# Performance work log

Hardware: AMD Instinct MI355X
Metric: run time of the kernel (lower is better)

Reference implementation:

```python
import jax, jax.numpy as jnp
import numpy as np

D, HID, NH, L, T, B = 512, 2048, 8, 4, 32, 16


def _pe(length, dim):
    pos = jnp.arange(length, dtype=jnp.float32)[:, None]
    div = jnp.exp(jnp.arange(0, dim, 2, dtype=jnp.float32) * (-np.log(10000.0) / dim))
    pe = jnp.zeros((length, dim), dtype=jnp.float32)
    pe = pe.at[:, 0::2].set(jnp.sin(pos * div)).at[:, 1::2].set(jnp.cos(pos * div))
    return pe[None]  # [1, length, dim]


def _ln(x, g, b, eps=1e-5):
    m = x.mean(-1, keepdims=True)
    v = ((x - m) ** 2).mean(-1, keepdims=True)
    return (x - m) * jax.lax.rsqrt(v + eps) * g + b


def _mha(xq, xkv, w, b, ow, ob):
    # torch MultiheadAttention: packed in_proj weight [3D, D], out_proj [D, D]
    d = xq.shape[-1]
    hd = d // NH
    q = xq @ w[:d].T + b[:d]
    k = xkv @ w[d:2 * d].T + b[d:2 * d]
    v = xkv @ w[2 * d:].T + b[2 * d:]
    sp = lambda t: t.reshape(t.shape[0], t.shape[1], NH, hd)
    att = jnp.einsum('bqhd,bkhd->bhqk', sp(q), sp(k)) / np.sqrt(hd)
    att = jax.nn.softmax(att, axis=-1)
    o = jnp.einsum('bhqk,bkhd->bqhd', att, sp(v))
    return o.reshape(o.shape[0], o.shape[1], d) @ ow.T + ob


def _ffn(x, w1, b1, w2, b2):
    return jax.nn.gelu(x @ w1.T + b1, approximate=False) @ w2.T + b2


def setup_inputs():
    key = jax.random.key(0)
    kit = iter(jax.random.split(key, 64))
    rn = lambda shape, s=0.02: jax.random.normal(next(kit), shape, dtype=jnp.float32) * s
    z = lambda shape: jnp.zeros(shape, jnp.float32)
    o = lambda shape: jnp.ones(shape, jnp.float32)
    inp = dict(y=jax.random.normal(next(kit), (B, D), dtype=jnp.float32),
               start_vec=rn((1, 1, D), 1.0), target_length=T)
    inp.update(enc_qkv_w=rn((L, 3 * D, D)), enc_qkv_b=z((L, 3 * D)), enc_out_w=rn((L, D, D)), enc_out_b=z((L, D)),
               enc_ff1_w=rn((L, HID, D)), enc_ff1_b=z((L, HID)), enc_ff2_w=rn((L, D, HID)), enc_ff2_b=z((L, D)),
               enc_ln1_g=o((L, D)), enc_ln1_b=z((L, D)), enc_ln2_g=o((L, D)), enc_ln2_b=z((L, D)),
               enc_lnf_g=o((D,)), enc_lnf_b=z((D,)),
               dec_qkv_w=rn((L, 3 * D, D)), dec_qkv_b=z((L, 3 * D)), dec_out_w=rn((L, D, D)), dec_out_b=z((L, D)),
               dec_x_qkv_w=rn((L, 3 * D, D)), dec_x_qkv_b=z((L, 3 * D)), dec_x_out_w=rn((L, D, D)), dec_x_out_b=z((L, D)),
               dec_ff1_w=rn((L, HID, D)), dec_ff1_b=z((L, HID)), dec_ff2_w=rn((L, D, HID)), dec_ff2_b=z((L, D)),
               dec_ln1_g=o((L, D)), dec_ln1_b=z((L, D)), dec_ln2_g=o((L, D)), dec_ln2_b=z((L, D)),
               dec_ln3_g=o((L, D)), dec_ln3_b=z((L, D)), dec_lnf_g=o((D,)), dec_lnf_b=z((D,)))
    return inp


def reference(y, start_vec, enc_qkv_w, enc_qkv_b, enc_out_w, enc_out_b, enc_ff1_w, enc_ff1_b, enc_ff2_w, enc_ff2_b,
              enc_ln1_g, enc_ln1_b, enc_ln2_g, enc_ln2_b, enc_lnf_g, enc_lnf_b,
              dec_qkv_w, dec_qkv_b, dec_out_w, dec_out_b, dec_x_qkv_w, dec_x_qkv_b, dec_x_out_w, dec_x_out_b,
              dec_ff1_w, dec_ff1_b, dec_ff2_w, dec_ff2_b,
              dec_ln1_g, dec_ln1_b, dec_ln2_g, dec_ln2_b, dec_ln3_g, dec_ln3_b, dec_lnf_g, dec_lnf_b,
              target_length):
    Bsz, Dm = y.shape
    pe = _pe(target_length, Dm)
    # encoder: src seq_len = 1; encoder output is identical every step, compute once
    x = y[:, None, :] + pe[:, :1]
    for i in range(L):
        x = _ln(x + _mha(x, x, enc_qkv_w[i], enc_qkv_b[i], enc_out_w[i], enc_out_b[i]), enc_ln1_g[i], enc_ln1_b[i])
        x = _ln(x + _ffn(x, enc_ff1_w[i], enc_ff1_b[i], enc_ff2_w[i], enc_ff2_b[i]), enc_ln2_g[i], enc_ln2_b[i])
    mem = _ln(x, enc_lnf_g, enc_lnf_b)
    tgt = jnp.tile(start_vec, (Bsz, 1, 1))
    for _ in range(target_length):
        h = tgt + pe[:, :tgt.shape[1]]
        for i in range(L):
            h = _ln(h + _mha(h, h, dec_qkv_w[i], dec_qkv_b[i], dec_out_w[i], dec_out_b[i]), dec_ln1_g[i], dec_ln1_b[i])
            h = _ln(h + _mha(h, mem, dec_x_qkv_w[i], dec_x_qkv_b[i], dec_x_out_w[i], dec_x_out_b[i]), dec_ln2_g[i], dec_ln2_b[i])
            h = _ln(h + _ffn(h, dec_ff1_w[i], dec_ff1_b[i], dec_ff2_w[i], dec_ff2_b[i]), dec_ln3_g[i], dec_ln3_b[i])
        h = _ln(h, dec_lnf_g, dec_lnf_b)
        tgt = jnp.concatenate([tgt, h[:, -1:, :]], axis=1)
    return tgt[:, 1:, :]
```

## Files before the change

### kernel.cpp

```cpp
#include <hip/hip_runtime.h>
#include <math.h>


#define NB 128
#define NT 512
#define GM 8
#define NGRP 16
#define Dm 512
#define HIDN 2048
#define TLEN 32
#define BSZ 16
#define NLAY 4
#define PBF 147968

typedef unsigned int uint32;
typedef unsigned short u16;
typedef short bf16x8 __attribute__((ext_vector_type(8)));
typedef float f32x4 __attribute__((ext_vector_type(4)));

struct Params {
  const float* y; const float* start;
  const float *eqw, *eqb, *eow, *eob, *ef1w, *ef1b, *ef2w, *ef2b;
  const float *eln1g, *eln1b, *eln2g, *eln2b, *elnfg, *elnfb;
  const float *dqw, *dqb, *dow, *dob, *dxqw, *dxqb, *dxow, *dxob;
  const float *df1w, *df1b, *df2w, *df2b;
  const float *dln1g, *dln1b, *dln2g, *dln2b, *dln3g, *dln3b, *dlnfg, *dlnfb;
  float* out; float* ws;
};

__device__ __forceinline__ u16 f2b(float x) {
  uint32 u = __float_as_uint(x);
  u += 0x7fffu + ((u >> 16) & 1u);
  return (u16)(u >> 16);
}
__device__ __forceinline__ float dot4f(float4 a, float4 b) {
  return a.x*b.x + a.y*b.y + a.z*b.z + a.w*b.w;
}

struct DecS {
  u16 P[8][512];
  u16 Ob[16][520];
  float Of[16][516];
};
struct EncS { float xn[2048]; };
union Smem { DecS d; EncS e; };

__device__ __forceinline__ void wave_ln(float v[8], const float* __restrict__ g,
                                        const float* __restrict__ bt, int cb) {
  float sum = 0.f, sq = 0.f;
#pragma unroll
  for (int q = 0; q < 8; ++q) { sum += v[q]; sq += v[q]*v[q]; }
#pragma unroll
  for (int m = 32; m; m >>= 1) { sum += __shfl_xor(sum, m, 64); sq += __shfl_xor(sq, m, 64); }
  float mean = sum * (1.f/Dm);
  float var  = sq  * (1.f/Dm) - mean*mean;
  float rs = rsqrtf(var + 1e-5f);
#pragma unroll
  for (int q = 0; q < 8; ++q) v[q] = (v[q]-mean)*rs*g[cb+q] + bt[cb+q];
}

template<int K>
__device__ __forceinline__ void wave_gemm(const u16* __restrict__ A,
                                          const u16* __restrict__ W, f32x4 acc[4]) {
  const int lane = threadIdx.x & 63;
  const int l15 = lane & 15, kg = lane >> 4;
  const u16* a = A + (size_t)l15*K + kg*8;
  const u16* w = W + (size_t)l15*K + kg*8;
#pragma unroll 4
  for (int kc = 0; kc < K/32; ++kc) {
    bf16x8 av = *(const bf16x8*)(a + kc*32);
#pragma unroll
    for (int cg = 0; cg < 4; ++cg) {
      bf16x8 bv = *(const bf16x8*)(w + (size_t)cg*16*K + kc*32);
      acc[cg] = __builtin_amdgcn_mfma_f32_16x16x32_bf16(av, bv, acc[cg], 0, 0, 0);
    }
  }
}

__device__ __forceinline__ float dotn(const float* __restrict__ xn,
                                      const float* __restrict__ w, int n4) {
  const float4* x4 = (const float4*)xn;
  const float4* w4 = (const float4*)w;
  float a = 0.f;
#pragma unroll 8
  for (int k = 0; k < n4; ++k) a += dot4f(x4[k], w4[k]);
  return a;
}

__device__ void convw(const float* __restrict__ s, u16* __restrict__ d, int n,
                      int gtid, int gs) {
  const float2* s2 = (const float2*)s;
  uint32* d2 = (uint32*)d;
  for (int i = gtid; i < n/2; i += gs) {
    float2 v = s2[i];
    d2[i] = (uint32)f2b(v.x) | ((uint32)f2b(v.y) << 16);
  }
}

#define BAR(cp, n, ep) do {                                                       \
    __syncthreads();                                                              \
    if (t == 0) {                                                                 \
      __hip_atomic_fetch_add((cp), 1u, __ATOMIC_RELEASE, __HIP_MEMORY_SCOPE_AGENT);\
      ++(ep);                                                                     \
      unsigned tg_ = (ep) * (unsigned)(n);                                        \
      while (__hip_atomic_load((cp), __ATOMIC_RELAXED, __HIP_MEMORY_SCOPE_AGENT) < tg_) \
        __builtin_amdgcn_s_sleep(2);                                              \
      (void)__hip_atomic_load((cp), __ATOMIC_ACQUIRE, __HIP_MEMORY_SCOPE_AGENT);  \
    }                                                                             \
    __syncthreads();                                                              \
  } while (0)

__global__ __launch_bounds__(NT) void ar_transformer(Params p) {
  __shared__ Smem sm;
  const int bid = blockIdx.x;
  const int t = threadIdx.x;
  const int g = bid & 15;
  const int m = bid >> 4;
  const int b = g;
  const int wv = t >> 6, lane = t & 63, cb = lane * 8;
  const int l15 = lane & 15, kg = lane >> 4;
  unsigned epA = 0, epG = 0;

  unsigned* cbase = (unsigned*)p.ws;
  unsigned* cntA = cbase;
  unsigned* cntG = cbase + 16 + g*16;
  float* f = p.ws + 1024;
  float* pe = f;            f += TLEN*Dm;
  float* batch0 = f;        f += (size_t)NGRP * PBF;
  u16* wq16 = (u16*)f;
  u16* wo16 = wq16 + (size_t)NLAY*1536*512;
  u16* w116 = wo16 + (size_t)NLAY*512*512;
  u16* w216 = w116 + (size_t)NLAY*2048*512;

  float* bb = batch0 + (size_t)b * PBF;
  float* xrow = bb, *arow = bb+512, *ofrow = bb+1024, *h2row = bb+1536, *frow = bb+2048;
  float* urow = bb+2560, *vxall = bb+4608, *crossE = bb+6656;
  float* h0f = bb+8704, *hf = bb+25088, *h2f = bb+41472;
  u16* ub16 = (u16*)(bb + 57856);
  u16* h0b  = ub16;
  u16* hb   = h0b + 16384;
  u16* h2b  = hb + 16384;
  u16* qkvb = h2b + 16384;
  u16* ubuf = qkvb + 49152;
  u16* vt   = ubuf + 65536;

  const int gtid = bid*NT + t, gs = NB*NT;

  convw(p.dqw,  wq16, NLAY*1536*512, gtid, gs);
  convw(p.dow,  wo16, NLAY*512*512,  gtid, gs);
  convw(p.df1w, w116, NLAY*2048*512, gtid, gs);
  convw(p.df2w, w216, NLAY*512*2048, gtid, gs);
  for (int i = gtid; i < TLEN*Dm; i += gs) {
    int tt = i >> 9, d = i & (Dm-1);
    int half = d >> 1;
    float ang = (float)tt * expf(-(float)(2*half) * (9.210340371976184f/512.0f));
    pe[i] = (d & 1) ? cosf(ang) : sinf(ang);
  }
  for (int i = gtid; i < BSZ*Dm; i += gs) {
    int bI = i >> 9, c = i & (Dm-1);
    float* bbI = batch0 + (size_t)bI*PBF;
    bbI[c] = p.y[i] + ((c & 1) ? 1.0f : 0.0f);
    float v0 = p.start[c] + ((c & 1) ? 1.0f : 0.0f);
    bbI[8704 + c] = v0;
    ((u16*)(bbI + 57856))[c] = f2b(v0);
  }
  BAR(cntA, NB, epA);

  for (int l = 0; l < NLAY; ++l) {
    if (l == 0) {
      for (int i = t; i < 512; i += NT) sm.e.xn[i] = xrow[i];
    } else if (wv == 0) {
      float v[8];
#pragma unroll
      for (int q = 0; q < 8; ++q) v[q] = h2row[cb+q] + frow[cb+q];
      wave_ln(v, p.eln2g + (l-1)*Dm, p.eln2b + (l-1)*Dm, cb);
#pragma unroll
      for (int q = 0; q < 8; ++q) sm.e.xn[cb+q] = v[q];
      if (m == 0)
#pragma unroll
        for (int q = 0; q < 8; ++q) xrow[cb+q] = v[q];
    }
    __syncthreads();
    if (t < 64) {
      int c = m*64 + t;
      arow[c] = dotn(sm.e.xn, p.eqw + ((size_t)l*1536 + 1024 + c)*512, 128)
                + p.eqb[l*1536 + 1024 + c];
    }
    BAR(cntG, GM, epG);
    for (int i = t; i < 512; i += NT) sm.e.xn[i] = arow[i];
    __syncthreads();
    if (t < 64) {
      int c = m*64 + t;
      ofrow[c] = dotn(sm.e.xn, p.eow + ((size_t)l*512 + c)*512, 128) + p.eob[l*512 + c];
    }
    BAR(cntG, GM, epG);
    if (wv == 0) {
      float v[8];
#pragma unroll
      for (int q = 0; q < 8; ++q) v[q] = xrow[cb+q] + ofrow[cb+q];
      wave_ln(v, p.eln1g + l*Dm, p.eln1b + l*Dm, cb);
#pragma unroll
      for (int q = 0; q < 8; ++q) sm.e.xn[cb+q] = v[q];
      if (m == 0)
#pragma unroll
        for (int q = 0; q < 8; ++q) h2row[cb+q] = v[q];
    }
    __syncthreads();
    if (t < 256) {
      int c = m*256 + t;
      float u = dotn(sm.e.xn, p.ef1w + ((size_t)l*2048 + c)*512, 128) + p.ef1b[l*2048 + c];
      u = 0.5f*u*(1.0f + erff(u*0.70710678118654752f));
      urow[c] = u;
    }
    BAR(cntG, GM, epG);
    for (int i = t; i < 2048; i += NT) sm.e.xn[i] = urow[i];
    __syncthreads();
    if (t < 64) {
      int c = m*64 + t;
      frow[c] = dotn(sm.e.xn, p.ef2w + ((size_t)l*512 + c)*2048, 512) + p.ef2b[l*512 + c];
    }
    BAR(cntG, GM, epG);
  }
  if (wv == 0) {
    float v[8];
#pragma unroll
    for (int q = 0; q < 8; ++q) v[q] = h2row[cb+q] + frow[cb+q];
    wave_ln(v, p.eln2g + 3*Dm, p.eln2b + 3*Dm, cb);
    wave_ln(v, p.elnfg, p.elnfb, cb);
#pragma unroll
    for (int q = 0; q < 8; ++q) sm.e.xn[cb+q] = v[q];
  }
  __syncthreads();
  if (t < 256) {
    int cc = m*256 + t, lc = cc >> 9, c = cc & 511;
    vxall[cc] = dotn(sm.e.xn, p.dxqw + ((size_t)lc*1536 + 1024 + c)*512, 128)
                + p.dxqb[lc*1536 + 1024 + c];
  }
  BAR(cntG, GM, epG);
  for (int i = t; i < 2048; i += NT) sm.e.xn[i] = vxall[i];
  __syncthreads();
  if (t < 256) {
    int cc = m*256 + t, lc = cc >> 9, c = cc & 511;
    crossE[cc] = dotn(sm.e.xn + lc*512, p.dxow + ((size_t)lc*512 + c)*512, 128)
                 + p.dxob[lc*512 + c];
  }
  BAR(cntG, GM, epG);

  for (int st = 0; st < TLEN; ++st) {
    const int s = st + 1;
    const int JT = (s + 15) >> 4;
    const int jtL = (s - 1) >> 4;
    for (int l = 0; l < NLAY; ++l) {
      {
        const u16* Asrc = (l == 0) ? h0b : hb;
        int ntile = JT*24, tid = m*8 + wv;
        if (tid < ntile) {
          int jt = tid/24, c24 = tid%24, c0 = c24*64;
          f32x4 acc[4] = {};
          wave_gemm<512>(Asrc + (size_t)jt*16*512, wq16 + ((size_t)l*1536 + c0)*512, acc);
#pragma unroll
          for (int cg = 0; cg < 4; ++cg) {
            int col = c0 + cg*16 + l15;
            float bias = p.dqb[l*1536 + col];
#pragma unroll
            for (int r = 0; r < 4; ++r) {
              int j = jt*16 + kg*4 + r;
              if (j < s) {
                float v = acc[cg][r] + bias;
                if (col < 512)       qkvb[(size_t)j*1536 + col] = f2b(v * 0.125f);
                else if (col < 1024) qkvb[(size_t)j*1536 + col] = f2b(v);
                else {
                  int d = col - 1024;
                  vt[(size_t)((d >> 6)*64 + (d & 63))*32 + j] = f2b(v);
                }
              }
            }
          }
        }
      }
      BAR(cntG, GM, epG);
      {
        bool act; int jt;
        if (l == NLAY-1) { act = (m == 0); jt = jtL; }
        else             { act = (m < JT); jt = m;   }
        if (act) {
          const int h = wv;
          f32x4 sc[2] = {};
          const u16* qA = qkvb + (size_t)(jt*16 + l15)*1536 + h*64 + kg*8;
          const u16* kB = qkvb + 512 + h*64 + kg*8;
#pragma unroll
          for (int ks = 0; ks < 2; ++ks) {
            bf16x8 av = *(const bf16x8*)(qA + ks*32);
#pragma unroll
            for (int cg = 0; cg < 2; ++cg) {
              bf16x8 bv = *(const bf16x8*)(kB + (size_t)(cg*16 + l15)*1536 + ks*32);
              sc[cg] = __builtin_amdgcn_mfma_f32_16x16x32_bf16(av, bv, sc[cg], 0, 0, 0);
            }
          }
#pragma unroll
          for (int r = 0; r < 4; ++r) {
            float v0 = (l15      < s) ? sc[0][r] : -3.0e38f;
            float v1 = (l15 + 16 < s) ? sc[1][r] : -3.0e38f;
            float mx = fmaxf(v0, v1);
#pragma unroll
            for (int mk = 1; mk < 16; mk <<= 1) mx = fmaxf(mx, __shfl_xor(mx, mk, 64));
            float e0 = expf(v0 - mx), e1 = expf(v1 - mx);
            float sum = e0 + e1;
#pragma unroll
            for (int mk = 1; mk < 16; mk <<= 1) sum += __shfl_xor(sum, mk, 64);
            float inv = 1.0f / sum;
            int row = kg*4 + r;
            sm.d.P[h][row*32 + l15]      = f2b(e0 * inv);
            sm.d.P[h][row*32 + 16 + l15] = f2b(e1 * inv);
          }
          __syncthreads();
          f32x4 ov[4] = {};
          bf16x8 pa = *(const bf16x8*)&sm.d.P[h][l15*32 + kg*8];
#pragma unroll
          for (int cg = 0; cg < 4; ++cg) {
            bf16x8 bv = *(const bf16x8*)(vt + (size_t)(h*64 + cg*16 + l15)*32 + kg*8);
            ov[cg] = __builtin_amdgcn_mfma_f32_16x16x32_bf16(pa, bv, ov[cg], 0, 0, 0);
          }
#pragma unroll
          for (int cg = 0; cg < 4; ++cg)
#pragma unroll
            for (int r = 0; r < 4; ++r)
              sm.d.Ob[kg*4 + r][h*64 + cg*16 + l15] = f2b(ov[cg][r]);
          __syncthreads();
          f32x4 oc[4] = {};
          int c0 = wv*64;
          const u16* wB = wo16 + ((size_t)l*512 + c0 + l15)*512 + kg*8;
#pragma unroll 4
          for (int ks = 0; ks < 16; ++ks) {
            bf16x8 av = *(const bf16x8*)&sm.d.Ob[l15][kg*8 + ks*32];
#pragma unroll
            for (int cg = 0; cg < 4; ++cg) {
              bf16x8 bv = *(const bf16x8*)(wB + (size_t)cg*16*512 + ks*32);
              oc[cg] = __builtin_amdgcn_mfma_f32_16x16x32_bf16(av, bv, oc[cg], 0, 0, 0);
            }
          }
#pragma unroll
          for (int cg = 0; cg < 4; ++cg) {
            int col = c0 + cg*16 + l15;
            float bias = p.dob[l*512 + col];
#pragma unroll
            for (int r = 0; r < 4; ++r)
              sm.d.Of[kg*4 + r][col] = oc[cg][r] + bias;
          }
          __syncthreads();
          const float* xin = (l == 0) ? h0f : hf;
          for (int jr = wv; jr < 16; jr += 8) {
            int j = jt*16 + jr;
            float v[8];
#pragma unroll
            for (int q = 0; q < 8; ++q) v[q] = xin[(size_t)j*512 + cb+q] + sm.d.Of[jr][cb+q];
            wave_ln(v, p.dln1g + l*512, p.dln1b + l*512, cb);
#pragma unroll
            for (int q = 0; q < 8; ++q) v[q] += crossE[l*512 + cb+q];
            wave_ln(v, p.dln2g + l*512, p.dln2b + l*512, cb);
            if (j < s) {
#pragma unroll
              for (int q = 0; q < 8; ++q) {
                h2f[(size_t)j*512 + cb+q] = v[q];
                h2b[(size_t)j*512 + cb+q] = f2b(v[q]);
              }
            }
          }
        }
      }
      BAR(cntG, GM, epG);
      {
        int ntile = (l == NLAY-1) ? 32 : JT*32;
        int tid = m*8 + wv;
        if (tid < ntile) {
          int jt, c;
          if (l == NLAY-1) { jt = jtL; c = tid; } else { jt = tid >> 5; c = tid & 31; }
          f32x4 acc[4] = {};
          wave_gemm<512>(h2b + (size_t)jt*16*512, w116 + ((size_t)l*2048 + c*64)*512, acc);
#pragma unroll
          for (int cg = 0; cg < 4; ++cg) {
            int col = c*64 + cg*16 + l15;
            float bias = p.df1b[l*2048 + col];
#pragma unroll
            for (int r = 0; r < 4; ++r) {
              int j = jt*16 + kg*4 + r;
              if (j < s) {
                float u = acc[cg][r] + bias;
                u = 0.5f*u*(1.0f + erff(u*0.70710678118654752f));
                ubuf[(size_t)j*2048 + col] = f2b(u);
              }
            }
          }
        }
      }
      BAR(cntG, GM, epG);
      {
        bool act; int jt;
        if (l == NLAY-1) { act = (m == 0); jt = jtL; }
        else             { act = (m < JT); jt = m;   }
        if (act) {
          f32x4 acc[4] = {};
          int c0 = wv*64;
          wave_gemm<2048>(ubuf + (size_t)jt*16*2048, w216 + ((size_t)l*512 + c0)*2048, acc);
#pragma unroll
          for (int cg = 0; cg < 4; ++cg) {
            int col = c0 + cg*16 + l15;
            float bias = p.df2b[l*512 + col];
#pragma unroll
            for (int r = 0; r < 4; ++r)
              sm.d.Of[kg*4 + r][col] = acc[cg][r] + bias;
          }
          __syncthreads();
          for (int jr = wv; jr < 16; jr += 8) {
            int j = jt*16 + jr;
            float v[8];
#pragma unroll
            for (int q = 0; q < 8; ++q) v[q] = h2f[(size_t)j*512 + cb+q] + sm.d.Of[jr][cb+q];
            wave_ln(v, p.dln3g + l*512, p.dln3b + l*512, cb);
            if (j < s) {
#pragma unroll
              for (int q = 0; q < 8; ++q) {
                hf[(size_t)j*512 + cb+q] = v[q];
                hb[(size_t)j*512 + cb+q] = f2b(v[q]);
              }
            }
            if (l == NLAY-1 && j == s-1) {
              wave_ln(v, p.dlnfg, p.dlnfb, cb);
#pragma unroll
              for (int q = 0; q < 8; ++q) {
                float ov = v[q];
                p.out[(size_t)(b*TLEN + st)*512 + cb+q] = ov;
                if (st + 1 < TLEN) {
                  float nh = ov + pe[(size_t)(st+1)*512 + cb+q];
                  h0f[(size_t)(st+1)*512 + cb+q] = nh;
                  h0b[(size_t)(st+1)*512 + cb+q] = f2b(nh);
                }
              }
            }
          }
        }
      }
      BAR(cntG, GM, epG);
    }
  }
}

extern "C" void kernel_launch(void* const* d_in, const int* in_sizes, int n_in,
                              void* d_out, int out_size, void* d_ws, size_t ws_size,
                              hipStream_t stream) {
  Params P;
  P.y     = (const float*)d_in[0];
  P.start = (const float*)d_in[1];
  P.eqw  = (const float*)d_in[3];  P.eqb  = (const float*)d_in[4];
  P.eow  = (const float*)d_in[5];  P.eob  = (const float*)d_in[6];
  P.ef1w = (const float*)d_in[7];  P.ef1b = (const float*)d_in[8];
  P.ef2w = (const float*)d_in[9];  P.ef2b = (const float*)d_in[10];
  P.eln1g = (const float*)d_in[11]; P.eln1b = (const float*)d_in[12];
  P.eln2g = (const float*)d_in[13]; P.eln2b = (const float*)d_in[14];
  P.elnfg = (const float*)d_in[15]; P.elnfb = (const float*)d_in[16];
  P.dqw  = (const float*)d_in[17]; P.dqb  = (const float*)d_in[18];
  P.dow  = (const float*)d_in[19]; P.dob  = (const float*)d_in[20];
  P.dxqw = (const float*)d_in[21]; P.dxqb = (const float*)d_in[22];
  P.dxow = (const float*)d_in[23]; P.dxob = (const float*)d_in[24];
  P.df1w = (const float*)d_in[25]; P.df1b = (const float*)d_in[26];
  P.df2w = (const float*)d_in[27]; P.df2b = (const float*)d_in[28];
  P.dln1g = (const float*)d_in[29]; P.dln1b = (const float*)d_in[30];
  P.dln2g = (const float*)d_in[31]; P.dln2b = (const float*)d_in[32];
  P.dln3g = (const float*)d_in[33]; P.dln3b = (const float*)d_in[34];
  P.dlnfg = (const float*)d_in[35]; P.dlnfb = (const float*)d_in[36];
  P.out = (float*)d_out;
  P.ws  = (float*)d_ws;
  hipMemsetAsync(d_ws, 0, 4096, stream);
  hipLaunchKernelGGL(ar_transformer, dim3(NB), dim3(NT), 0, stream, P);
}
```

Baseline: 22.31 ms.

## Run one 1024-thread block per batch row and drop inter-block grid barriers

The kernel moves from 128 blocks (8 cooperating blocks per batch row, synchronized with atomic counter barriers) to 16 blocks of 1024 threads, one per batch row. All per-step stages then sync with __syncthreads only. The GEMM helper is changed so each wave handles two 16-row tiles, and the FFN intermediate is kept in LDS. This removes the cost of the global barriers but uses an eighth as many CUs, so the weight GEMMs lose a lot of parallelism and each block has to stream all the weights by itself.

```diff
diff --git a/kernel.cpp b/kernel.cpp
--- a/kernel.cpp
+++ b/kernel.cpp
@@ -2,16 +2,13 @@
 #include <math.h>
 
 
-#define NB 128
-#define NT 512
-#define GM 8
-#define NGRP 16
+#define NBLK 16
+#define NT 1024
 #define Dm 512
 #define HIDN 2048
 #define TLEN 32
-#define BSZ 16
 #define NLAY 4
-#define PBF 147968
+#define RSZ 149504
 
 typedef unsigned int uint32;
 typedef unsigned short u16;
@@ -37,12 +34,8 @@
   return a.x*b.x + a.y*b.y + a.z*b.z + a.w*b.w;
 }
 
-struct DecS {
-  u16 P[8][512];
-  u16 Ob[16][520];
-  float Of[16][516];
-};
-struct EncS { float xn[2048]; };
+struct DecS { u16 P[16][16][32]; u16 u[2][16][2056]; };
+struct EncS { float xs[512]; float as[512]; float h2[512]; float fr[512]; float us[2048]; };
 union Smem { DecS d; EncS e; };
 
 __device__ __forceinline__ void wave_ln(float v[8], const float* __restrict__ g,
@@ -60,19 +53,22 @@
 }
 
 template<int K>
-__device__ __forceinline__ void wave_gemm(const u16* __restrict__ A,
-                                          const u16* __restrict__ W, f32x4 acc[4]) {
+__device__ __forceinline__ void wgemm2(const u16* __restrict__ A, int lda, int nj,
+                                       const u16* __restrict__ W, f32x4 acc[2][4]) {
   const int lane = threadIdx.x & 63;
   const int l15 = lane & 15, kg = lane >> 4;
-  const u16* a = A + (size_t)l15*K + kg*8;
-  const u16* w = W + (size_t)l15*K + kg*8;
-#pragma unroll 4
+  const u16* a0 = A + (size_t)l15*lda + kg*8;
+  const u16* a1 = a0 + (size_t)(nj > 1 ? 16 : 0)*lda;
+#pragma unroll 2
   for (int kc = 0; kc < K/32; ++kc) {
-    bf16x8 av = *(const bf16x8*)(a + kc*32);
+    bf16x8 av0 = *(const bf16x8*)(a0 + kc*32);
+    bf16x8 av1 = *(const bf16x8*)(a1 + kc*32);
+    const u16* w = W + (size_t)l15*K + kg*8 + kc*32;
 #pragma unroll
     for (int cg = 0; cg < 4; ++cg) {
-      bf16x8 bv = *(const bf16x8*)(w + (size_t)cg*16*K + kc*32);
-      acc[cg] = __builtin_amdgcn_mfma_f32_16x16x32_bf16(av, bv, acc[cg], 0, 0, 0);
+      bf16x8 bv = *(const bf16x8*)(w + (size_t)cg*16*K);
+      acc[0][cg] = __builtin_amdgcn_mfma_f32_16x16x32_bf16(av0, bv, acc[0][cg], 0, 0, 0);
+      acc[1][cg] = __builtin_amdgcn_mfma_f32_16x16x32_bf16(av1, bv, acc[1][cg], 0, 0, 0);
     }
   }
 }
@@ -97,194 +93,160 @@
   }
 }
 
-#define BAR(cp, n, ep) do {                                                       \
-    __syncthreads();                                                              \
-    if (t == 0) {                                                                 \
-      __hip_atomic_fetch_add((cp), 1u, __ATOMIC_RELEASE, __HIP_MEMORY_SCOPE_AGENT);\
-      ++(ep);                                                                     \
-      unsigned tg_ = (ep) * (unsigned)(n);                                        \
-      while (__hip_atomic_load((cp), __ATOMIC_RELAXED, __HIP_MEMORY_SCOPE_AGENT) < tg_) \
-        __builtin_amdgcn_s_sleep(2);                                              \
-      (void)__hip_atomic_load((cp), __ATOMIC_ACQUIRE, __HIP_MEMORY_SCOPE_AGENT);  \
-    }                                                                             \
-    __syncthreads();                                                              \
-  } while (0)
-
 __global__ __launch_bounds__(NT) void ar_transformer(Params p) {
   __shared__ Smem sm;
   const int bid = blockIdx.x;
+  const int b = bid;
   const int t = threadIdx.x;
-  const int g = bid & 15;
-  const int m = bid >> 4;
-  const int b = g;
   const int wv = t >> 6, lane = t & 63, cb = lane * 8;
   const int l15 = lane & 15, kg = lane >> 4;
-  unsigned epA = 0, epG = 0;
-
-  unsigned* cbase = (unsigned*)p.ws;
-  unsigned* cntA = cbase;
-  unsigned* cntG = cbase + 16 + g*16;
-  float* f = p.ws + 1024;
-  float* pe = f;            f += TLEN*Dm;
-  float* batch0 = f;        f += (size_t)NGRP * PBF;
-  u16* wq16 = (u16*)f;
+
+  unsigned* cnt = (unsigned*)p.ws;
+  u16* wq16 = (u16*)(p.ws + 256);
   u16* wo16 = wq16 + (size_t)NLAY*1536*512;
   u16* w116 = wo16 + (size_t)NLAY*512*512;
   u16* w216 = w116 + (size_t)NLAY*2048*512;
-
-  float* bb = batch0 + (size_t)b * PBF;
-  float* xrow = bb, *arow = bb+512, *ofrow = bb+1024, *h2row = bb+1536, *frow = bb+2048;
-  float* urow = bb+2560, *vxall = bb+4608, *crossE = bb+6656;
-  float* h0f = bb+8704, *hf = bb+25088, *h2f = bb+41472;
-  u16* ub16 = (u16*)(bb + 57856);
-  u16* h0b  = ub16;
+  float* bat0 = (float*)(w216 + (size_t)NLAY*512*2048);
+
+  float* bb   = bat0 + (size_t)b * RSZ;
+  float* pe   = bb;
+  float* h0f  = bb + 16384;
+  float* hf   = bb + 32768;
+  float* h2f  = bb + 49152;
+  float* ofb  = bb + 65536;
+  float* crossE = bb + 81920;
+  u16* h0b  = (u16*)(bb + 83968);
   u16* hb   = h0b + 16384;
   u16* h2b  = hb + 16384;
   u16* qkvb = h2b + 16384;
-  u16* ubuf = qkvb + 49152;
-  u16* vt   = ubuf + 65536;
-
-  const int gtid = bid*NT + t, gs = NB*NT;
+  u16* vt   = qkvb + 49152;
+  u16* obb  = vt + 16384;
+
+  const int gtid = bid*NT + t, gs = NBLK*NT;
 
   convw(p.dqw,  wq16, NLAY*1536*512, gtid, gs);
   convw(p.dow,  wo16, NLAY*512*512,  gtid, gs);
   convw(p.df1w, w116, NLAY*2048*512, gtid, gs);
   convw(p.df2w, w216, NLAY*512*2048, gtid, gs);
-  for (int i = gtid; i < TLEN*Dm; i += gs) {
+  for (int i = t; i < TLEN*Dm; i += NT) {
     int tt = i >> 9, d = i & (Dm-1);
     int half = d >> 1;
     float ang = (float)tt * expf(-(float)(2*half) * (9.210340371976184f/512.0f));
     pe[i] = (d & 1) ? cosf(ang) : sinf(ang);
   }
-  for (int i = gtid; i < BSZ*Dm; i += gs) {
-    int bI = i >> 9, c = i & (Dm-1);
-    float* bbI = batch0 + (size_t)bI*PBF;
-    bbI[c] = p.y[i] + ((c & 1) ? 1.0f : 0.0f);
-    float v0 = p.start[c] + ((c & 1) ? 1.0f : 0.0f);
-    bbI[8704 + c] = v0;
-    ((u16*)(bbI + 57856))[c] = f2b(v0);
-  }
-  BAR(cntA, NB, epA);
+  if (t < 512) {
+    float v0 = p.start[t] + ((t & 1) ? 1.0f : 0.0f);
+    h0f[t] = v0; h0b[t] = f2b(v0);
+  }
+  __syncthreads();
+  if (t == 0) {
+    __hip_atomic_fetch_add(cnt, 1u, __ATOMIC_RELEASE, __HIP_MEMORY_SCOPE_AGENT);
+    while (__hip_atomic_load(cnt, __ATOMIC_RELAXED, __HIP_MEMORY_SCOPE_AGENT) < (unsigned)NBLK)
+      __builtin_amdgcn_s_sleep(2);
+    (void)__hip_atomic_load(cnt, __ATOMIC_ACQUIRE, __HIP_MEMORY_SCOPE_AGENT);
+  }
+  __syncthreads();
 
   for (int l = 0; l < NLAY; ++l) {
     if (l == 0) {
-      for (int i = t; i < 512; i += NT) sm.e.xn[i] = xrow[i];
+      if (t < 512) sm.e.xs[t] = p.y[(size_t)b*512 + t] + ((t & 1) ? 1.0f : 0.0f);
     } else if (wv == 0) {
       float v[8];
 #pragma unroll
-      for (int q = 0; q < 8; ++q) v[q] = h2row[cb+q] + frow[cb+q];
+      for (int q = 0; q < 8; ++q) v[q] = sm.e.h2[cb+q] + sm.e.fr[cb+q];
       wave_ln(v, p.eln2g + (l-1)*Dm, p.eln2b + (l-1)*Dm, cb);
 #pragma unroll
-      for (int q = 0; q < 8; ++q) sm.e.xn[cb+q] = v[q];
-      if (m == 0)
-#pragma unroll
-        for (int q = 0; q < 8; ++q) xrow[cb+q] = v[q];
+      for (int q = 0; q < 8; ++q) sm.e.xs[cb+q] = v[q];
     }
     __syncthreads();
-    if (t < 64) {
-      int c = m*64 + t;
-      arow[c] = dotn(sm.e.xn, p.eqw + ((size_t)l*1536 + 1024 + c)*512, 128)
-                + p.eqb[l*1536 + 1024 + c];
-    }
-    BAR(cntG, GM, epG);
-    for (int i = t; i < 512; i += NT) sm.e.xn[i] = arow[i];
-    __syncthreads();
-    if (t < 64) {
-      int c = m*64 + t;
-      ofrow[c] = dotn(sm.e.xn, p.eow + ((size_t)l*512 + c)*512, 128) + p.eob[l*512 + c];
-    }
-    BAR(cntG, GM, epG);
+    if (t < 512)
+      sm.e.as[t] = dotn(sm.e.xs, p.eqw + ((size_t)l*1536 + 1024 + t)*512, 128)
+                   + p.eqb[l*1536 + 1024 + t];
+    __syncthreads();
+    if (t < 512)
+      sm.e.fr[t] = dotn(sm.e.as, p.eow + ((size_t)l*512 + t)*512, 128) + p.eob[l*512 + t];
+    __syncthreads();
     if (wv == 0) {
       float v[8];
 #pragma unroll
-      for (int q = 0; q < 8; ++q) v[q] = xrow[cb+q] + ofrow[cb+q];
+      for (int q = 0; q < 8; ++q) v[q] = sm.e.xs[cb+q] + sm.e.fr[cb+q];
       wave_ln(v, p.eln1g + l*Dm, p.eln1b + l*Dm, cb);
 #pragma unroll
-      for (int q = 0; q < 8; ++q) sm.e.xn[cb+q] = v[q];
-      if (m == 0)
-#pragma unroll
-        for (int q = 0; q < 8; ++q) h2row[cb+q] = v[q];
+      for (int q = 0; q < 8; ++q) sm.e.h2[cb+q] = v[q];
     }
     __syncthreads();
-    if (t < 256) {
-      int c = m*256 + t;
-      float u = dotn(sm.e.xn, p.ef1w + ((size_t)l*2048 + c)*512, 128) + p.ef1b[l*2048 + c];
-      u = 0.5f*u*(1.0f + erff(u*0.70710678118654752f));
-      urow[c] = u;
+    for (int c = t; c < 2048; c += NT) {
+      float u = dotn(sm.e.h2, p.ef1w + ((size_t)l*2048 + c)*512, 128) + p.ef1b[l*2048 + c];
+      sm.e.us[c] = 0.5f*u*(1.0f + erff(u*0.70710678118654752f));
     }
-    BAR(cntG, GM, epG);
-    for (int i = t; i < 2048; i += NT) sm.e.xn[i] = urow[i];
-    __syncthreads();
-    if (t < 64) {
-      int c = m*64 + t;
-      frow[c] = dotn(sm.e.xn, p.ef2w + ((size_t)l*512 + c)*2048, 512) + p.ef2b[l*512 + c];
-    }
-    BAR(cntG, GM, epG);
+    __syncthreads();
+    if (t < 512)
+      sm.e.fr[t] = dotn(sm.e.us, p.ef2w + ((size_t)l*512 + t)*2048, 512) + p.ef2b[l*512 + t];
+    __syncthreads();
   }
   if (wv == 0) {
     float v[8];
 #pragma unroll
-    for (int q = 0; q < 8; ++q) v[q] = h2row[cb+q] + frow[cb+q];
+    for (int q = 0; q < 8; ++q) v[q] = sm.e.h2[cb+q] + sm.e.fr[cb+q];
     wave_ln(v, p.eln2g + 3*Dm, p.eln2b + 3*Dm, cb);
     wave_ln(v, p.elnfg, p.elnfb, cb);
 #pragma unroll
-    for (int q = 0; q < 8; ++q) sm.e.xn[cb+q] = v[q];
+    for (int q = 0; q < 8; ++q) sm.e.xs[cb+q] = v[q];
   }
   __syncthreads();
-  if (t < 256) {
-    int cc = m*256 + t, lc = cc >> 9, c = cc & 511;
-    vxall[cc] = dotn(sm.e.xn, p.dxqw + ((size_t)lc*1536 + 1024 + c)*512, 128)
-                + p.dxqb[lc*1536 + 1024 + c];
-  }
-  BAR(cntG, GM, epG);
-  for (int i = t; i < 2048; i += NT) sm.e.xn[i] = vxall[i];
+  for (int c = t; c < 2048; c += NT) {
+    int lc = c >> 9, cc = c & 511;
+    sm.e.us[c] = dotn(sm.e.xs, p.dxqw + ((size_t)lc*1536 + 1024 + cc)*512, 128)
+                 + p.dxqb[lc*1536 + 1024 + cc];
+  }
   __syncthreads();
-  if (t < 256) {
-    int cc = m*256 + t, lc = cc >> 9, c = cc & 511;
-    crossE[cc] = dotn(sm.e.xn + lc*512, p.dxow + ((size_t)lc*512 + c)*512, 128)
-                 + p.dxob[lc*512 + c];
-  }
-  BAR(cntG, GM, epG);
+  for (int c = t; c < 2048; c += NT) {
+    int lc = c >> 9, cc = c & 511;
+    crossE[c] = dotn(sm.e.us + lc*512, p.dxow + ((size_t)lc*512 + cc)*512, 128)
+                + p.dxob[lc*512 + cc];
+  }
+  __syncthreads();
 
   for (int st = 0; st < TLEN; ++st) {
     const int s = st + 1;
     const int JT = (s + 15) >> 4;
     const int jtL = (s - 1) >> 4;
     for (int l = 0; l < NLAY; ++l) {
-      {
-        const u16* Asrc = (l == 0) ? h0b : hb;
-        int ntile = JT*24, tid = m*8 + wv;
-        if (tid < ntile) {
-          int jt = tid/24, c24 = tid%24, c0 = c24*64;
-          f32x4 acc[4] = {};
-          wave_gemm<512>(Asrc + (size_t)jt*16*512, wq16 + ((size_t)l*1536 + c0)*512, acc);
+      const int RT0 = (l == NLAY-1) ? jtL : 0;
+      const int RN  = (l == NLAY-1) ? 1 : JT;
+      const u16* Asrc = (l == 0) ? h0b : hb;
+
+      for (int it = wv; it < 24; it += 16) {
+        int c0 = it*64;
+        f32x4 acc[2][4];
+#pragma unroll
+        for (int a2 = 0; a2 < 2; ++a2)
+#pragma unroll
+          for (int cg = 0; cg < 4; ++cg) acc[a2][cg] = (f32x4){0.f,0.f,0.f,0.f};
+        wgemm2<512>(Asrc, 512, JT, wq16 + ((size_t)l*1536 + c0)*512, acc);
+        for (int jl = 0; jl < JT; ++jl)
 #pragma unroll
           for (int cg = 0; cg < 4; ++cg) {
             int col = c0 + cg*16 + l15;
             float bias = p.dqb[l*1536 + col];
 #pragma unroll
             for (int r = 0; r < 4; ++r) {
-              int j = jt*16 + kg*4 + r;
+              int j = jl*16 + kg*4 + r;
               if (j < s) {
-                float v = acc[cg][r] + bias;
+                float v = acc[jl][cg][r] + bias;
                 if (col < 512)       qkvb[(size_t)j*1536 + col] = f2b(v * 0.125f);
                 else if (col < 1024) qkvb[(size_t)j*1536 + col] = f2b(v);
-                else {
-                  int d = col - 1024;
-                  vt[(size_t)((d >> 6)*64 + (d & 63))*32 + j] = f2b(v);
-                }
+                else                 vt[(size_t)(col-1024)*32 + j] = f2b(v);
               }
             }
           }
-        }
-      }
-      BAR(cntG, GM, epG);
+      }
+      __syncthreads();
+
       {
-        bool act; int jt;
-        if (l == NLAY-1) { act = (m == 0); jt = jtL; }
-        else             { act = (m < JT); jt = m;   }
+        bool act = wv < 8*RN;
+        int h = wv & 7, jt = RT0 + (wv >> 3);
         if (act) {
-          const int h = wv;
           f32x4 sc[2] = {};
           const u16* qA = qkvb + (size_t)(jt*16 + l15)*1536 + h*64 + kg*8;
           const u16* kB = qkvb + 512 + h*64 + kg*8;
@@ -310,12 +272,11 @@
             for (int mk = 1; mk < 16; mk <<= 1) sum += __shfl_xor(sum, mk, 64);
             float inv = 1.0f / sum;
             int row = kg*4 + r;
-            sm.d.P[h][row*32 + l15]      = f2b(e0 * inv);
-            sm.d.P[h][row*32 + 16 + l15] = f2b(e1 * inv);
-          }
-          __syncthreads();
+            sm.d.P[wv][row][l15]      = f2b(e0 * inv);
+            sm.d.P[wv][row][16 + l15] = f2b(e1 * inv);
+          }
           f32x4 ov[4] = {};
-          bf16x8 pa = *(const bf16x8*)&sm.d.P[h][l15*32 + kg*8];
+          bf16x8 pa = *(const bf16x8*)&sm.d.P[wv][l15][kg*8];
 #pragma unroll
           for (int cg = 0; cg < 4; ++cg) {
             bf16x8 bv = *(const bf16x8*)(vt + (size_t)(h*64 + cg*16 + l15)*32 + kg*8);
@@ -325,122 +286,121 @@
           for (int cg = 0; cg < 4; ++cg)
 #pragma unroll
             for (int r = 0; r < 4; ++r)
-              sm.d.Ob[kg*4 + r][h*64 + cg*16 + l15] = f2b(ov[cg][r]);
-          __syncthreads();
-          f32x4 oc[4] = {};
-          int c0 = wv*64;
-          const u16* wB = wo16 + ((size_t)l*512 + c0 + l15)*512 + kg*8;
-#pragma unroll 4
-          for (int ks = 0; ks < 16; ++ks) {
-            bf16x8 av = *(const bf16x8*)&sm.d.Ob[l15][kg*8 + ks*32];
-#pragma unroll
-            for (int cg = 0; cg < 4; ++cg) {
-              bf16x8 bv = *(const bf16x8*)(wB + (size_t)cg*16*512 + ks*32);
-              oc[cg] = __builtin_amdgcn_mfma_f32_16x16x32_bf16(av, bv, oc[cg], 0, 0, 0);
+              obb[(size_t)(jt*16 + kg*4 + r)*512 + h*64 + cg*16 + l15] = f2b(ov[cg][r]);
+        }
+      }
+      __syncthreads();
+
+      for (int it = wv; it < 8*RN; it += 16) {
+        int c0 = (it & 7)*64, jt = RT0 + (it >> 3);
+        f32x4 acc[2][4];
+#pragma unroll
+        for (int a2 = 0; a2 < 2; ++a2)
+#pragma unroll
+          for (int cg = 0; cg < 4; ++cg) acc[a2][cg] = (f32x4){0.f,0.f,0.f,0.f};
+        wgemm2<512>(obb + (size_t)jt*16*512, 512, 1, wo16 + ((size_t)l*512 + c0)*512, acc);
+#pragma unroll
+        for (int cg = 0; cg < 4; ++cg) {
+          int col = c0 + cg*16 + l15;
+          float bias = p.dob[l*512 + col];
+#pragma unroll
+          for (int r = 0; r < 4; ++r)
+            ofb[(size_t)(jt*16 + kg*4 + r)*512 + col] = acc[0][cg][r] + bias;
+        }
+      }
+      __syncthreads();
+
+      {
+        const float* xin = (l == 0) ? h0f : hf;
+        for (int r = wv; r < RN*16; r += 16) {
+          int j = RT0*16 + r;
+          float v[8];
+#pragma unroll
+          for (int q = 0; q < 8; ++q) v[q] = xin[(size_t)j*512 + cb+q] + ofb[(size_t)j*512 + cb+q];
+          wave_ln(v, p.dln1g + l*512, p.dln1b + l*512, cb);
+#pragma unroll
+          for (int q = 0; q < 8; ++q) v[q] += crossE[l*512 + cb+q];
+          wave_ln(v, p.dln2g + l*512, p.dln2b + l*512, cb);
+          if (j < s) {
+#pragma unroll
+            for (int q = 0; q < 8; ++q) {
+              h2f[(size_t)j*512 + cb+q] = v[q];
+              h2b[(size_t)j*512 + cb+q] = f2b(v[q]);
             }
           }
+        }
+      }
+      __syncthreads();
+
+      for (int it = wv; it < 32; it += 16) {
+        int c0 = it*64;
+        f32x4 acc[2][4];
+#pragma unroll
+        for (int a2 = 0; a2 < 2; ++a2)
+#pragma unroll
+          for (int cg = 0; cg < 4; ++cg) acc[a2][cg] = (f32x4){0.f,0.f,0.f,0.f};
+        wgemm2<512>(h2b + (size_t)RT0*16*512, 512, RN, w116 + ((size_t)l*2048 + c0)*512, acc);
+        for (int jl = 0; jl < RN; ++jl)
 #pragma unroll
           for (int cg = 0; cg < 4; ++cg) {
             int col = c0 + cg*16 + l15;
-            float bias = p.dob[l*512 + col];
-#pragma unroll
-            for (int r = 0; r < 4; ++r)
-              sm.d.Of[kg*4 + r][col] = oc[cg][r] + bias;
-          }
-          __syncthreads();
-          const float* xin = (l == 0) ? h0f : hf;
-          for (int jr = wv; jr < 16; jr += 8) {
-            int j = jt*16 + jr;
-            float v[8];
-#pragma unroll
-            for (int q = 0; q < 8; ++q) v[q] = xin[(size_t)j*512 + cb+q] + sm.d.Of[jr][cb+q];
-            wave_ln(v, p.dln1g + l*512, p.dln1b + l*512, cb);
-#pragma unroll
-            for (int q = 0; q < 8; ++q) v[q] += crossE[l*512 + cb+q];
-            wave_ln(v, p.dln2g + l*512, p.dln2b + l*512, cb);
-            if (j < s) {
-#pragma unroll
-              for (int q = 0; q < 8; ++q) {
-                h2f[(size_t)j*512 + cb+q] = v[q];
-                h2b[(size_t)j*512 + cb+q] = f2b(v[q]);
-              }
+            float bias = p.df1b[l*2048 + col];
+#pragma unroll
+            for (int r = 0; r < 4; ++r) {
+              float u = acc[jl][cg][r] + bias;
+              sm.d.u[jl][kg*4 + r][col] = f2b(0.5f*u*(1.0f + erff(u*0.70710678118654752f)));
             }
           }
-        }
-      }
-      BAR(cntG, GM, epG);
-      {
-        int ntile = (l == NLAY-1) ? 32 : JT*32;
-        int tid = m*8 + wv;
-        if (tid < ntile) {
-          int jt, c;
-          if (l == NLAY-1) { jt = jtL; c = tid; } else { jt = tid >> 5; c = tid & 31; }
-          f32x4 acc[4] = {};
-          wave_gemm<512>(h2b + (size_t)jt*16*512, w116 + ((size_t)l*2048 + c*64)*512, acc);
-#pragma unroll
-          for (int cg = 0; cg < 4; ++cg) {
-            int col = c*64 + cg*16 + l15;
-            float bias = p.df1b[l*2048 + col];
-#pragma unroll
-            for (int r = 0; r < 4; ++r) {
-              int j = jt*16 + kg*4 + r;
-              if (j < s) {
-                float u = acc[cg][r] + bias;
-                u = 0.5f*u*(1.0f + erff(u*0.70710678118654752f));
-                ubuf[(size_t)j*2048 + col] = f2b(u);
-              }
-            }
-          }
-        }
-      }
-      BAR(cntG, GM, epG);
-      {
-        bool act; int jt;
-        if (l == NLAY-1) { act = (m == 0); jt = jtL; }
-        else             { act = (m < JT); jt = m;   }
-        if (act) {
-          f32x4 acc[4] = {};
-          int c0 = wv*64;
-          wave_gemm<2048>(ubuf + (size_t)jt*16*2048, w216 + ((size_t)l*512 + c0)*2048, acc);
+      }
+      __syncthreads();
+      for (int it = wv; it < 8; it += 16) {
+        int c0 = it*64;
+        f32x4 acc[2][4];
+#pragma unroll
+        for (int a2 = 0; a2 < 2; ++a2)
+#pragma unroll
+          for (int cg = 0; cg < 4; ++cg) acc[a2][cg] = (f32x4){0.f,0.f,0.f,0.f};
+        wgemm2<2048>((const u16*)&sm.d.u[0][0][0], 2056, RN, w216 + ((size_t)l*512 + c0)*2048, acc);
+        for (int jl = 0; jl < RN; ++jl)
 #pragma unroll
           for (int cg = 0; cg < 4; ++cg) {
             int col = c0 + cg*16 + l15;
             float bias = p.df2b[l*512 + col];
 #pragma unroll
             for (int r = 0; r < 4; ++r)
-              sm.d.Of[kg*4 + r][col] = acc[cg][r] + bias;
-          }
-          __syncthreads();
-          for (int jr = wv; jr < 16; jr += 8) {
-            int j = jt*16 + jr;
-            float v[8];
-#pragma unroll
-            for (int q = 0; q < 8; ++q) v[q] = h2f[(size_t)j*512 + cb+q] + sm.d.Of[jr][cb+q];
-            wave_ln(v, p.dln3g + l*512, p.dln3b + l*512, cb);
-            if (j < s) {
-#pragma unroll
-              for (int q = 0; q < 8; ++q) {
-                hf[(size_t)j*512 + cb+q] = v[q];
-                hb[(size_t)j*512 + cb+q] = f2b(v[q]);
-              }
+              ofb[(size_t)(RT0*16 + jl*16 + kg*4 + r)*512 + col] = acc[jl][cg][r] + bias;
+          }
+      }
+      __syncthreads();
+
+      for (int r = wv; r < RN*16; r += 16) {
+        int j = RT0*16 + r;
+        float v[8];
+#pragma unroll
+        for (int q = 0; q < 8; ++q) v[q] = h2f[(size_t)j*512 + cb+q] + ofb[(size_t)j*512 + cb+q];
+        wave_ln(v, p.dln3g + l*512, p.dln3b + l*512, cb);
+        if (j < s) {
+#pragma unroll
+          for (int q = 0; q < 8; ++q) {
+            hf[(size_t)j*512 + cb+q] = v[q];
+            hb[(size_t)j*512 + cb+q] = f2b(v[q]);
+          }
+        }
+        if (l == NLAY-1 && j == s-1) {
+          wave_ln(v, p.dlnfg, p.dlnfb, cb);
+#pragma unroll
+          for (int q = 0; q < 8; ++q) {
+            float ov = v[q];
+            p.out[(size_t)(b*TLEN + st)*512 + cb+q] = ov;
+            if (st + 1 < TLEN) {
+              float nh = ov + pe[(size_t)(st+1)*512 + cb+q];
+              h0f[(size_t)(st+1)*512 + cb+q] = nh;
+              h0b[(size_t)(st+1)*512 + cb+q] = f2b(nh);
             }
-            if (l == NLAY-1 && j == s-1) {
-              wave_ln(v, p.dlnfg, p.dlnfb, cb);
-#pragma unroll
-              for (int q = 0; q < 8; ++q) {
-                float ov = v[q];
-                p.out[(size_t)(b*TLEN + st)*512 + cb+q] = ov;
-                if (st + 1 < TLEN) {
-                  float nh = ov + pe[(size_t)(st+1)*512 + cb+q];
-                  h0f[(size_t)(st+1)*512 + cb+q] = nh;
-                  h0b[(size_t)(st+1)*512 + cb+q] = f2b(nh);
-                }
-              }
-            }
           }
         }
       }
-      BAR(cntG, GM, epG);
+      __syncthreads();
     }
   }
 }
@@ -470,6 +430,6 @@
   P.dlnfg = (const float*)d_in[35]; P.dlnfb = (const float*)d_in[36];
   P.out = (float*)d_out;
   P.ws  = (float*)d_ws;
-  hipMemsetAsync(d_ws, 0, 4096, stream);
-  hipLaunchKernelGGL(ar_transformer, dim3(NB), dim3(NT), 0, stream, P);
-}
+  hipMemsetAsync(d_ws, 0, 1024, stream);
+  hipLaunchKernelGGL(ar_transformer, dim3(NBLK), dim3(NT), 0, stream, P);
+}
```

Result: slower. 37.86 ms (+69.7%).
